# Kernel optimization log

Hardware: AMD Instinct MI355X
Metric: run time of the kernel (lower is better)

Reference implementation:

```python
import jax, jax.numpy as jnp
import numpy as np

B, S, H, I, E, TOPK = 4, 4096, 1024, 4096, 8, 2


def setup_inputs() -> dict:
    key = jax.random.key(0)
    k0, k1, k2, k3 = jax.random.split(key, 4)
    hidden_states = jax.random.normal(k0, (B, S, H), dtype=jnp.float32)
    # Router gate: Linear(hidden_size -> num_experts), no bias
    Wg = jax.random.normal(k1, (E, H), dtype=jnp.float32) * 0.02
    # Stacked per-expert FeedForward: w2(silu(w1(x)))
    W1 = jax.random.normal(k2, (E, I, H), dtype=jnp.float32) * 0.02
    b1 = jnp.zeros((E, I), dtype=jnp.float32)
    W2 = jax.random.normal(k3, (E, H, I), dtype=jnp.float32) * 0.02
    b2 = jnp.zeros((E, H), dtype=jnp.float32)
    return {"hidden_states": hidden_states, "Wg": Wg, "W1": W1, "b1": b1, "W2": W2, "b2": b2}


def _moe_forward(x, Wg, W1, b1, W2, b2):
    b, s, h = x.shape
    # Router: logits [B,S,E], softmax over experts, top-k, renormalize top-k weights
    logits = jnp.einsum("bsh,eh->bse", x, Wg)
    probs = jax.nn.softmax(logits, axis=-1)
    vals, idx = jax.lax.top_k(probs, TOPK)                      # [B,S,K]
    vals = vals / jnp.sum(vals, axis=-1, keepdims=True)
    # Dense combine weights [B,S,E] (E is small); zero for non-selected experts
    combine = jnp.sum(jax.nn.one_hot(idx, E, dtype=x.dtype) * vals[..., None], axis=-2)

    xf = x.reshape(b * s, h)                                    # [T,H]
    gate_te = combine.reshape(b * s, E).T                       # [E,T]

    def body(acc, xs):
        W1e, b1e, W2e, b2e, ge = xs
        hmid = jax.nn.silu(xf @ W1e.T + b1e)                    # [T,I]
        oe = hmid @ W2e.T + b2e                                 # [T,H]
        return acc + ge[:, None] * oe, None

    out, _ = jax.lax.scan(body, jnp.zeros_like(xf), (W1, b1, W2, b2, gate_te))
    return out.reshape(b, s, h), logits


def reference(hidden_states, Wg, W1, b1, W2, b2):
    return _moe_forward(hidden_states, Wg, W1, b1, W2, b2)
```

## Files before the change

### kernel.cpp

```cpp
#include <hip/hip_runtime.h>
#include <hip/hip_bf16.h>
#include <stdint.h>

#define T_TOK 16384
#define HDIM  1024
#define IDIM  4096
#define NEXP  8

typedef __bf16  bf16x8  __attribute__((ext_vector_type(8)));
typedef float   floatx4 __attribute__((ext_vector_type(4)));

__device__ __forceinline__ void gload16(const void* g, void* lds) {
  __builtin_amdgcn_global_load_lds(
      (__attribute__((address_space(1))) void*)g,
      (__attribute__((address_space(3))) void*)lds, 16, 0, 0);
}

__global__ __launch_bounds__(256) void cvtk(const float* __restrict__ s,
                                            __bf16* __restrict__ d, int n8) {
  int i = blockIdx.x * 256 + threadIdx.x;
  if (i >= n8) return;
  const float4* s4 = (const float4*)s;
  float4 a = s4[2 * i], b = s4[2 * i + 1];
  bf16x8 v;
  v[0] = (__bf16)a.x; v[1] = (__bf16)a.y; v[2] = (__bf16)a.z; v[3] = (__bf16)a.w;
  v[4] = (__bf16)b.x; v[5] = (__bf16)b.y; v[6] = (__bf16)b.z; v[7] = (__bf16)b.w;
  *(bf16x8*)(d + (size_t)i * 8) = v;
}

__global__ __launch_bounds__(256) void routerk(const float* __restrict__ x,
    const float* __restrict__ Wg, float* __restrict__ logits,
    int* __restrict__ topk_e, float* __restrict__ topk_g,
    int* __restrict__ gcount) {
  __shared__ int hist[NEXP];
  int tid = threadIdx.x;
  if (tid < NEXP) hist[tid] = 0;
  __syncthreads();
  int wv = tid >> 6, ln = tid & 63;
  for (int it = 0; it < 16; ++it) {
    int t = blockIdx.x * 64 + wv * 16 + it;
    const float* xr = x + (size_t)t * HDIM;
    float acc[NEXP];
#pragma unroll
    for (int e = 0; e < NEXP; e++) acc[e] = 0.f;
    for (int h = ln; h < HDIM; h += 64) {
      float xv = xr[h];
#pragma unroll
      for (int e = 0; e < NEXP; e++) acc[e] += xv * Wg[e * HDIM + h];
    }
#pragma unroll
    for (int e = 0; e < NEXP; e++) {
#pragma unroll
      for (int off = 32; off > 0; off >>= 1) acc[e] += __shfl_down(acc[e], off);
    }
    if (ln == 0) {
#pragma unroll
      for (int e = 0; e < NEXP; e++) logits[(size_t)t * NEXP + e] = acc[e];
      int i0 = 0;
#pragma unroll
      for (int e = 1; e < NEXP; e++) if (acc[e] > acc[i0]) i0 = e;
      int i1 = (i0 == 0) ? 1 : 0;
#pragma unroll
      for (int e = 0; e < NEXP; e++)
        if (e != i0 && e != i1 && acc[e] > acc[i1]) i1 = e;
      float r = expf(acc[i1] - acc[i0]);
      float s = 1.f + r;
      topk_e[2 * t] = i0;     topk_g[2 * t] = 1.f / s;
      topk_e[2 * t + 1] = i1; topk_g[2 * t + 1] = r / s;
      atomicAdd(&hist[i0], 1);
      atomicAdd(&hist[i1], 1);
    }
  }
  __syncthreads();
  if (tid < NEXP) atomicAdd(&gcount[tid], hist[tid]);
}

__global__ void prefixk(const int* __restrict__ gcount, int* __restrict__ goff,
                        int* __restrict__ gcur, int* __restrict__ tbl,
                        int* __restrict__ ntb, int CH) {
  if (threadIdx.x != 0 || blockIdx.x != 0) return;
  int s = 0;
  for (int g = 0; g < NEXP; g++) { goff[g] = s; gcur[g] = s; s += gcount[g]; }
  goff[NEXP] = s;
  int chunk_rows = (2 * T_TOK) / CH;
  int cnt[16];
  for (int c = 0; c < CH; c++) cnt[c] = 0;
  for (int g = 0; g < NEXP; g++) {
    int Ne = goff[g + 1] - goff[g];
    int nb = (Ne + 127) >> 7;
    for (int b = 0; b < nb; b++) {
      int gr0 = goff[g] + b * 128;
      int c = gr0 / chunk_rows;
      tbl[c * 288 + cnt[c]] = (g << 8) | b;
      cnt[c]++;
    }
  }
  for (int c = 0; c < CH; c++) ntb[c] = cnt[c];
}

__global__ __launch_bounds__(256) void scatterk(const int* __restrict__ topk_e,
    const float* __restrict__ topk_g, int* __restrict__ gcur,
    int* __restrict__ row_info, float* __restrict__ row_gate) {
  __shared__ int hist[NEXP];
  __shared__ int bbase[NEXP];
  int tid = threadIdx.x;
  if (tid < NEXP) hist[tid] = 0;
  __syncthreads();
  int t = blockIdx.x * 256 + tid;
  int e0 = topk_e[2 * t], e1 = topk_e[2 * t + 1];
  float g0 = topk_g[2 * t], g1 = topk_g[2 * t + 1];
  int l0 = atomicAdd(&hist[e0], 1);
  int l1 = atomicAdd(&hist[e1], 1);
  __syncthreads();
  if (tid < NEXP) bbase[tid] = atomicAdd(&gcur[tid], hist[tid]);
  __syncthreads();
  int p0 = bbase[e0] + l0;
  row_info[p0] = t; row_gate[p0] = g0;
  int p1 = bbase[e1] + l1;
  row_info[p1] = t; row_gate[p1] = g1;
}

__global__ __launch_bounds__(256) void gemm1k(
    const __bf16* __restrict__ xb, const __bf16* __restrict__ w1b,
    const float* __restrict__ b1, __bf16* __restrict__ hmid,
    const int* __restrict__ row_info, const int* __restrict__ goff,
    const int* __restrict__ tbl, const int* __restrict__ ntb, int chunk_base) {
  __shared__ __attribute__((aligned(16))) char smem[32768];
  if ((int)blockIdx.x >= ntb[0]) return;
  int info = tbl[blockIdx.x];
  int g = info >> 8, br = info & 255;
  int base = goff[g];
  int Ne = goff[g + 1] - base;
  int r0 = br * 128;
  if (r0 >= Ne) return;
  int n0 = blockIdx.y * 128;
  int tid = threadIdx.x, w = tid >> 6, ln = tid & 63;
  int ra = w * 32 + (ln >> 2);
  int ca = (ln & 3) * 16;
  int rA0 = r0 + ra;      if (rA0 > Ne - 1) rA0 = Ne - 1;
  int rA1 = r0 + ra + 16; if (rA1 > Ne - 1) rA1 = Ne - 1;
  int t0 = row_info[base + rA0];
  int t1 = row_info[base + rA1];
  const char* gA0 = (const char*)(xb + (size_t)t0 * HDIM) + ca;
  const char* gA1 = (const char*)(xb + (size_t)t1 * HDIM) + ca;
  const char* gB0 = (const char*)(w1b + (size_t)g * IDIM * HDIM + (size_t)(n0 + ra) * HDIM) + ca;
  const char* gB1 = (const char*)(w1b + (size_t)g * IDIM * HDIM + (size_t)(n0 + ra + 16) * HDIM) + ca;
  int aoff = w * 2048;
  int boff = 8192 + w * 2048;
  int lm = ln & 15, lq = ln >> 4;
  int rdA = ((w >> 1) * 64 + lm) * 64 + lq * 16;
  int rdB = 8192 + ((w & 1) * 64 + lm) * 64 + lq * 16;
  floatx4 acc[4][4] = {};
  gload16(gA0, smem + aoff);
  gload16(gA1, smem + aoff + 1024);
  gload16(gB0, smem + boff);
  gload16(gB1, smem + boff + 1024);
  const int NK = HDIM / 32;
  for (int kt = 0; kt < NK; kt++) {
    char* cbuf = smem + (kt & 1) * 16384;
    char* nbuf = smem + ((kt + 1) & 1) * 16384;
    __syncthreads();
    if (kt + 1 < NK) {
      int kb = (kt + 1) * 64;
      gload16(gA0 + kb, nbuf + aoff);
      gload16(gA1 + kb, nbuf + aoff + 1024);
      gload16(gB0 + kb, nbuf + boff);
      gload16(gB1 + kb, nbuf + boff + 1024);
    }
    bf16x8 af[4], bfv[4];
#pragma unroll
    for (int mi = 0; mi < 4; mi++) af[mi] = *(const bf16x8*)(cbuf + rdA + mi * 1024);
#pragma unroll
    for (int ni = 0; ni < 4; ni++) bfv[ni] = *(const bf16x8*)(cbuf + rdB + ni * 1024);
#pragma unroll
    for (int mi = 0; mi < 4; mi++)
#pragma unroll
      for (int ni = 0; ni < 4; ni++)
        acc[mi][ni] = __builtin_amdgcn_mfma_f32_16x16x32_bf16(af[mi], bfv[ni], acc[mi][ni], 0, 0, 0);
  }
  int colbase = n0 + (w & 1) * 64;
#pragma unroll
  for (int mi = 0; mi < 4; mi++) {
#pragma unroll
    for (int reg = 0; reg < 4; reg++) {
      int rr = r0 + (w >> 1) * 64 + mi * 16 + lq * 4 + reg;
      if (rr < Ne) {
        __bf16* orow = hmid + (size_t)(base + rr - chunk_base) * IDIM;
#pragma unroll
        for (int ni = 0; ni < 4; ni++) {
          int c = colbase + ni * 16 + lm;
          float v = acc[mi][ni][reg] + b1[g * IDIM + c];
          v = v / (1.f + __expf(-v));
          orow[c] = (__bf16)v;
        }
      }
    }
  }
}

__global__ __launch_bounds__(256) void gemm2k(
    const __bf16* __restrict__ hmid, const __bf16* __restrict__ w2b,
    const float* __restrict__ b2, float* __restrict__ out,
    const int* __restrict__ row_info, const float* __restrict__ row_gate,
    const int* __restrict__ goff, const int* __restrict__ tbl,
    const int* __restrict__ ntb, int chunk_base) {
  __shared__ __attribute__((aligned(16))) char smem[32768];
  if ((int)blockIdx.x >= ntb[0]) return;
  int info = tbl[blockIdx.x];
  int g = info >> 8, br = info & 255;
  int base = goff[g];
  int Ne = goff[g + 1] - base;
  int r0 = br * 128;
  if (r0 >= Ne) return;
  int n0 = blockIdx.y * 128;
  int tid = threadIdx.x, w = tid >> 6, ln = tid & 63;
  int ra = w * 32 + (ln >> 2);
  int ca = (ln & 3) * 16;
  int rA0 = r0 + ra;      if (rA0 > Ne - 1) rA0 = Ne - 1;
  int rA1 = r0 + ra + 16; if (rA1 > Ne - 1) rA1 = Ne - 1;
  const char* gA0 = (const char*)(hmid + (size_t)(base + rA0 - chunk_base) * IDIM) + ca;
  const char* gA1 = (const char*)(hmid + (size_t)(base + rA1 - chunk_base) * IDIM) + ca;
  const char* gB0 = (const char*)(w2b + (size_t)g * HDIM * IDIM + (size_t)(n0 + ra) * IDIM) + ca;
  const char* gB1 = (const char*)(w2b + (size_t)g * HDIM * IDIM + (size_t)(n0 + ra + 16) * IDIM) + ca;
  int aoff = w * 2048;
  int boff = 8192 + w * 2048;
  int lm = ln & 15, lq = ln >> 4;
  int rdA = ((w >> 1) * 64 + lm) * 64 + lq * 16;
  int rdB = 8192 + ((w & 1) * 64 + lm) * 64 + lq * 16;
  floatx4 acc[4][4] = {};
  gload16(gA0, smem + aoff);
  gload16(gA1, smem + aoff + 1024);
  gload16(gB0, smem + boff);
  gload16(gB1, smem + boff + 1024);
  const int NK = IDIM / 32;
  for (int kt = 0; kt < NK; kt++) {
    char* cbuf = smem + (kt & 1) * 16384;
    char* nbuf = smem + ((kt + 1) & 1) * 16384;
    __syncthreads();
    if (kt + 1 < NK) {
      int kb = (kt + 1) * 64;
      gload16(gA0 + kb, nbuf + aoff);
      gload16(gA1 + kb, nbuf + aoff + 1024);
      gload16(gB0 + kb, nbuf + boff);
      gload16(gB1 + kb, nbuf + boff + 1024);
    }
    bf16x8 af[4], bfv[4];
#pragma unroll
    for (int mi = 0; mi < 4; mi++) af[mi] = *(const bf16x8*)(cbuf + rdA + mi * 1024);
#pragma unroll
    for (int ni = 0; ni < 4; ni++) bfv[ni] = *(const bf16x8*)(cbuf + rdB + ni * 1024);
#pragma unroll
    for (int mi = 0; mi < 4; mi++)
#pragma unroll
      for (int ni = 0; ni < 4; ni++)
        acc[mi][ni] = __builtin_amdgcn_mfma_f32_16x16x32_bf16(af[mi], bfv[ni], acc[mi][ni], 0, 0, 0);
  }
  int colbase = n0 + (w & 1) * 64;
#pragma unroll
  for (int mi = 0; mi < 4; mi++) {
#pragma unroll
    for (int reg = 0; reg < 4; reg++) {
      int rr = r0 + (w >> 1) * 64 + mi * 16 + lq * 4 + reg;
      if (rr < Ne) {
        int t = row_info[base + rr];
        float gate = row_gate[base + rr];
        float* orow = out + (size_t)t * HDIM;
#pragma unroll
        for (int ni = 0; ni < 4; ni++) {
          int c = colbase + ni * 16 + lm;
          float v = gate * (acc[mi][ni][reg] + b2[g * HDIM + c]);
          atomicAdd(&orow[c], v);
        }
      }
    }
  }
}

extern "C" void kernel_launch(void* const* d_in, const int* in_sizes, int n_in,
                              void* d_out, int out_size, void* d_ws, size_t ws_size,
                              hipStream_t stream) {
  (void)in_sizes; (void)n_in; (void)out_size;
  const float* x  = (const float*)d_in[0];
  const float* Wg = (const float*)d_in[1];
  const float* W1 = (const float*)d_in[2];
  const float* b1 = (const float*)d_in[3];
  const float* W2 = (const float*)d_in[4];
  const float* b2 = (const float*)d_in[5];
  float* out = (float*)d_out;
  float* logits = out + (size_t)T_TOK * HDIM;

  const size_t xb_b   = (size_t)T_TOK * HDIM * 2;
  const size_t w_b    = (size_t)NEXP * IDIM * HDIM * 2;
  const size_t side_b = (size_t)2 * T_TOK * 4;
  const size_t meta_b = 32768;
  int CH = 2;
  while (CH < 16) {
    size_t hm = ((size_t)((2 * T_TOK) / CH) + 128) * IDIM * 2;
    size_t need = xb_b + 2 * w_b + hm + 4 * side_b + meta_b + 8192;
    if (need <= ws_size) break;
    CH *= 2;
  }
  const int R = (2 * T_TOK) / CH;

  char* p = (char*)d_ws;
  size_t off = 0;
  auto take = [&](size_t bytes) -> char* {
    char* r = p + off;
    off = (off + bytes + 255) & ~(size_t)255;
    return r;
  };
  __bf16* xb   = (__bf16*)take(xb_b);
  __bf16* w1b  = (__bf16*)take(w_b);
  __bf16* w2b  = (__bf16*)take(w_b);
  __bf16* hmid = (__bf16*)take(((size_t)R + 128) * IDIM * 2);
  int*   topk_e   = (int*)take(side_b);
  float* topk_g   = (float*)take(side_b);
  int*   row_info = (int*)take(side_b);
  float* row_gate = (float*)take(side_b);
  int*   gcount   = (int*)take(16 * 4);
  int*   goff     = (int*)take(17 * 4);
  int*   gcur     = (int*)take(16 * 4);
  int*   ntb      = (int*)take(16 * 4);
  int*   tbl      = (int*)take(16 * 288 * 4);

  hipMemsetAsync(gcount, 0, 16 * 4, stream);
  hipMemsetAsync(out, 0, (size_t)T_TOK * HDIM * 4, stream);

  cvtk<<<(T_TOK * HDIM / 8) / 256, 256, 0, stream>>>(x, xb, T_TOK * HDIM / 8);
  cvtk<<<(NEXP * IDIM * HDIM / 8) / 256, 256, 0, stream>>>(W1, w1b, NEXP * IDIM * HDIM / 8);
  cvtk<<<(NEXP * IDIM * HDIM / 8) / 256, 256, 0, stream>>>(W2, w2b, NEXP * IDIM * HDIM / 8);
  routerk<<<T_TOK / 64, 256, 0, stream>>>(x, Wg, logits, topk_e, topk_g, gcount);
  prefixk<<<1, 64, 0, stream>>>(gcount, goff, gcur, tbl, ntb, CH);
  scatterk<<<T_TOK / 256, 256, 0, stream>>>(topk_e, topk_g, gcur, row_info, row_gate);

  int gx = R / 128 + 8;
  for (int c = 0; c < CH; c++) {
    gemm1k<<<dim3(gx, IDIM / 128, 1), 256, 0, stream>>>(
        xb, w1b, b1, hmid, row_info, goff, tbl + c * 288, ntb + c, c * R);
    gemm2k<<<dim3(gx, HDIM / 128, 1), 256, 0, stream>>>(
        hmid, w2b, b2, out, row_info, row_gate, goff, tbl + c * 288, ntb + c, c * R);
  }
}
```

Measured before the change: 1.519 ms.

## Enlarge MoE GEMM tiles to 256x256 with 4-stage swizzled LDS pipeline

```diff
diff --git a/kernel.cpp b/kernel.cpp
--- a/kernel.cpp
+++ b/kernel.cpp
@@ -87,9 +87,9 @@
   for (int c = 0; c < CH; c++) cnt[c] = 0;
   for (int g = 0; g < NEXP; g++) {
     int Ne = goff[g + 1] - goff[g];
-    int nb = (Ne + 127) >> 7;
+    int nb = (Ne + 255) >> 8;
     for (int b = 0; b < nb; b++) {
-      int gr0 = goff[g] + b * 128;
+      int gr0 = goff[g] + b * 256;
       int c = gr0 / chunk_rows;
       tbl[c * 288 + cnt[c]] = (g << 8) | b;
       cnt[c]++;
@@ -120,70 +120,102 @@
   row_info[p1] = t; row_gate[p1] = g1;
 }
 
-__global__ __launch_bounds__(256) void gemm1k(
+
+__global__ __launch_bounds__(512, 2) void gemm1k(
     const __bf16* __restrict__ xb, const __bf16* __restrict__ w1b,
     const float* __restrict__ b1, __bf16* __restrict__ hmid,
     const int* __restrict__ row_info, const int* __restrict__ goff,
     const int* __restrict__ tbl, const int* __restrict__ ntb, int chunk_base) {
-  __shared__ __attribute__((aligned(16))) char smem[32768];
+  __shared__ __attribute__((aligned(16))) char smem[131072];
   if ((int)blockIdx.x >= ntb[0]) return;
   int info = tbl[blockIdx.x];
   int g = info >> 8, br = info & 255;
   int base = goff[g];
   int Ne = goff[g + 1] - base;
-  int r0 = br * 128;
+  int r0 = br * 256;
   if (r0 >= Ne) return;
-  int n0 = blockIdx.y * 128;
-  int tid = threadIdx.x, w = tid >> 6, ln = tid & 63;
-  int ra = w * 32 + (ln >> 2);
-  int ca = (ln & 3) * 16;
-  int rA0 = r0 + ra;      if (rA0 > Ne - 1) rA0 = Ne - 1;
-  int rA1 = r0 + ra + 16; if (rA1 > Ne - 1) rA1 = Ne - 1;
-  int t0 = row_info[base + rA0];
-  int t1 = row_info[base + rA1];
-  const char* gA0 = (const char*)(xb + (size_t)t0 * HDIM) + ca;
-  const char* gA1 = (const char*)(xb + (size_t)t1 * HDIM) + ca;
-  const char* gB0 = (const char*)(w1b + (size_t)g * IDIM * HDIM + (size_t)(n0 + ra) * HDIM) + ca;
-  const char* gB1 = (const char*)(w1b + (size_t)g * IDIM * HDIM + (size_t)(n0 + ra + 16) * HDIM) + ca;
-  int aoff = w * 2048;
-  int boff = 8192 + w * 2048;
+  int n0 = blockIdx.y * 256;
+  int tid = threadIdx.x, wid = tid >> 6, ln = tid & 63;
+  int wm = wid >> 2, wn = wid & 3;
   int lm = ln & 15, lq = ln >> 4;
-  int rdA = ((w >> 1) * 64 + lm) * 64 + lq * 16;
-  int rdB = 8192 + ((w & 1) * 64 + lm) * 64 + lq * 16;
-  floatx4 acc[4][4] = {};
-  gload16(gA0, smem + aoff);
-  gload16(gA1, smem + aoff + 1024);
-  gload16(gB0, smem + boff);
-  gload16(gB1, smem + boff + 1024);
-  const int NK = HDIM / 32;
-  for (int kt = 0; kt < NK; kt++) {
-    char* cbuf = smem + (kt & 1) * 16384;
-    char* nbuf = smem + ((kt + 1) & 1) * 16384;
-    __syncthreads();
-    if (kt + 1 < NK) {
-      int kb = (kt + 1) * 64;
-      gload16(gA0 + kb, nbuf + aoff);
-      gload16(gA1 + kb, nbuf + aoff + 1024);
-      gload16(gB0 + kb, nbuf + boff);
-      gload16(gB1 + kb, nbuf + boff + 1024);
-    }
-    bf16x8 af[4], bfv[4];
-#pragma unroll
-    for (int mi = 0; mi < 4; mi++) af[mi] = *(const bf16x8*)(cbuf + rdA + mi * 1024);
-#pragma unroll
-    for (int ni = 0; ni < 4; ni++) bfv[ni] = *(const bf16x8*)(cbuf + rdB + ni * 1024);
-#pragma unroll
-    for (int mi = 0; mi < 4; mi++)
-#pragma unroll
-      for (int ni = 0; ni < 4; ni++)
-        acc[mi][ni] = __builtin_amdgcn_mfma_f32_16x16x32_bf16(af[mi], bfv[ni], acc[mi][ni], 0, 0, 0);
-  }
-  int colbase = n0 + (w & 1) * 64;
-#pragma unroll
-  for (int mi = 0; mi < 4; mi++) {
+
+  int rb = tid >> 2;
+  int srcs = ((tid & 3) ^ ((tid >> 3) & 3)) * 16;
+  const char* gA[2]; const char* gB[2];
+#pragma unroll
+  for (int r = 0; r < 2; r++) {
+    int row = r0 + r * 128 + rb;
+    int rc = row < Ne ? row : Ne - 1;
+    int tk = row_info[base + rc];
+    gA[r] = (const char*)(xb + (size_t)tk * HDIM) + srcs;
+    gB[r] = (const char*)(w1b + (size_t)g * IDIM * HDIM +
+                          (size_t)(n0 + r * 128 + rb) * HDIM) + srcs;
+  }
+  int swz = (lq ^ ((lm >> 1) & 3)) * 16;
+  int rdA = (wm * 128 + lm) * 64 + swz;
+  int rdB = 16384 + (wn * 64 + lm) * 64 + swz;
+
+  floatx4 acc[8][4] = {};
+
+#define STAGE_A1(T) { int b_ = (T) & 3; size_t ko = (size_t)(T) * 64; \
+    gload16(gA[0] + ko, smem + b_ * 32768 + tid * 16); \
+    gload16(gA[1] + ko, smem + b_ * 32768 + 8192 + tid * 16); }
+#define STAGE_B1(T) { int b_ = (T) & 3; size_t ko = (size_t)(T) * 64; \
+    gload16(gB[0] + ko, smem + b_ * 32768 + 16384 + tid * 16); \
+    gload16(gB[1] + ko, smem + b_ * 32768 + 24576 + tid * 16); }
+
+  const int NT = HDIM / 32;
+#pragma unroll
+  for (int p = 0; p < 3; p++) { STAGE_A1(p); STAGE_B1(p); }
+
+#pragma unroll 1
+  for (int t = 0; t < NT; t++) {
+    bool st = (t < NT - 3);
+    if (st) STAGE_A1(t + 3);
+    int rem = NT - 1 - t;
+    if (rem >= 3)      asm volatile("s_waitcnt vmcnt(10)" ::: "memory");
+    else if (rem == 2) asm volatile("s_waitcnt vmcnt(8)" ::: "memory");
+    else if (rem == 1) asm volatile("s_waitcnt vmcnt(4)" ::: "memory");
+    else               asm volatile("s_waitcnt vmcnt(0)" ::: "memory");
+    __builtin_amdgcn_s_barrier();
+    asm volatile("" ::: "memory");
+    const char* cb = smem + (t & 3) * 32768;
+    bf16x8 af[8], bf[2];
+#pragma unroll
+    for (int mi = 0; mi < 8; mi++) af[mi] = *(const bf16x8*)(cb + rdA + mi * 1024);
+#pragma unroll
+    for (int ni = 0; ni < 2; ni++) bf[ni] = *(const bf16x8*)(cb + rdB + ni * 1024);
+    __builtin_amdgcn_s_setprio(1);
+#pragma unroll
+    for (int mi = 0; mi < 8; mi++)
+#pragma unroll
+      for (int ni = 0; ni < 2; ni++)
+        acc[mi][ni] = __builtin_amdgcn_mfma_f32_16x16x32_bf16(af[mi], bf[ni], acc[mi][ni], 0, 0, 0);
+    __builtin_amdgcn_s_setprio(0);
+    if (st) STAGE_B1(t + 3);
+    bf16x8 bg[2];
+#pragma unroll
+    for (int ni = 0; ni < 2; ni++) bg[ni] = *(const bf16x8*)(cb + rdB + (2 + ni) * 1024);
+    __builtin_amdgcn_s_setprio(1);
+#pragma unroll
+    for (int mi = 0; mi < 8; mi++)
+#pragma unroll
+      for (int ni = 0; ni < 2; ni++)
+        acc[mi][2 + ni] = __builtin_amdgcn_mfma_f32_16x16x32_bf16(af[mi], bg[ni], acc[mi][2 + ni], 0, 0, 0);
+    __builtin_amdgcn_s_setprio(0);
+    asm volatile("" ::: "memory");
+    __builtin_amdgcn_s_barrier();
+    asm volatile("" ::: "memory");
+  }
+#undef STAGE_A1
+#undef STAGE_B1
+
+  int colbase = n0 + wn * 64;
+#pragma unroll
+  for (int mi = 0; mi < 8; mi++) {
 #pragma unroll
     for (int reg = 0; reg < 4; reg++) {
-      int rr = r0 + (w >> 1) * 64 + mi * 16 + lq * 4 + reg;
+      int rr = r0 + wm * 128 + mi * 16 + lq * 4 + reg;
       if (rr < Ne) {
         __bf16* orow = hmid + (size_t)(base + rr - chunk_base) * IDIM;
 #pragma unroll
@@ -198,69 +230,100 @@
   }
 }
 
-__global__ __launch_bounds__(256) void gemm2k(
+__global__ __launch_bounds__(512, 2) void gemm2k(
     const __bf16* __restrict__ hmid, const __bf16* __restrict__ w2b,
     const float* __restrict__ b2, float* __restrict__ out,
     const int* __restrict__ row_info, const float* __restrict__ row_gate,
     const int* __restrict__ goff, const int* __restrict__ tbl,
     const int* __restrict__ ntb, int chunk_base) {
-  __shared__ __attribute__((aligned(16))) char smem[32768];
+  __shared__ __attribute__((aligned(16))) char smem[131072];
   if ((int)blockIdx.x >= ntb[0]) return;
   int info = tbl[blockIdx.x];
   int g = info >> 8, br = info & 255;
   int base = goff[g];
   int Ne = goff[g + 1] - base;
-  int r0 = br * 128;
+  int r0 = br * 256;
   if (r0 >= Ne) return;
-  int n0 = blockIdx.y * 128;
-  int tid = threadIdx.x, w = tid >> 6, ln = tid & 63;
-  int ra = w * 32 + (ln >> 2);
-  int ca = (ln & 3) * 16;
-  int rA0 = r0 + ra;      if (rA0 > Ne - 1) rA0 = Ne - 1;
-  int rA1 = r0 + ra + 16; if (rA1 > Ne - 1) rA1 = Ne - 1;
-  const char* gA0 = (const char*)(hmid + (size_t)(base + rA0 - chunk_base) * IDIM) + ca;
-  const char* gA1 = (const char*)(hmid + (size_t)(base + rA1 - chunk_base) * IDIM) + ca;
-  const char* gB0 = (const char*)(w2b + (size_t)g * HDIM * IDIM + (size_t)(n0 + ra) * IDIM) + ca;
-  const char* gB1 = (const char*)(w2b + (size_t)g * HDIM * IDIM + (size_t)(n0 + ra + 16) * IDIM) + ca;
-  int aoff = w * 2048;
-  int boff = 8192 + w * 2048;
+  int n0 = blockIdx.y * 256;
+  int tid = threadIdx.x, wid = tid >> 6, ln = tid & 63;
+  int wm = wid >> 2, wn = wid & 3;
   int lm = ln & 15, lq = ln >> 4;
-  int rdA = ((w >> 1) * 64 + lm) * 64 + lq * 16;
-  int rdB = 8192 + ((w & 1) * 64 + lm) * 64 + lq * 16;
-  floatx4 acc[4][4] = {};
-  gload16(gA0, smem + aoff);
-  gload16(gA1, smem + aoff + 1024);
-  gload16(gB0, smem + boff);
-  gload16(gB1, smem + boff + 1024);
-  const int NK = IDIM / 32;
-  for (int kt = 0; kt < NK; kt++) {
-    char* cbuf = smem + (kt & 1) * 16384;
-    char* nbuf = smem + ((kt + 1) & 1) * 16384;
-    __syncthreads();
-    if (kt + 1 < NK) {
-      int kb = (kt + 1) * 64;
-      gload16(gA0 + kb, nbuf + aoff);
-      gload16(gA1 + kb, nbuf + aoff + 1024);
-      gload16(gB0 + kb, nbuf + boff);
-      gload16(gB1 + kb, nbuf + boff + 1024);
-    }
-    bf16x8 af[4], bfv[4];
-#pragma unroll
-    for (int mi = 0; mi < 4; mi++) af[mi] = *(const bf16x8*)(cbuf + rdA + mi * 1024);
-#pragma unroll
-    for (int ni = 0; ni < 4; ni++) bfv[ni] = *(const bf16x8*)(cbuf + rdB + ni * 1024);
-#pragma unroll
-    for (int mi = 0; mi < 4; mi++)
-#pragma unroll
-      for (int ni = 0; ni < 4; ni++)
-        acc[mi][ni] = __builtin_amdgcn_mfma_f32_16x16x32_bf16(af[mi], bfv[ni], acc[mi][ni], 0, 0, 0);
-  }
-  int colbase = n0 + (w & 1) * 64;
-#pragma unroll
-  for (int mi = 0; mi < 4; mi++) {
+
+  int rb = tid >> 2;
+  int srcs = ((tid & 3) ^ ((tid >> 3) & 3)) * 16;
+  const char* gA[2]; const char* gB[2];
+#pragma unroll
+  for (int r = 0; r < 2; r++) {
+    int row = r0 + r * 128 + rb;
+    gA[r] = (const char*)(hmid + (size_t)(base + row - chunk_base) * IDIM) + srcs;
+    gB[r] = (const char*)(w2b + (size_t)g * HDIM * IDIM +
+                          (size_t)(n0 + r * 128 + rb) * IDIM) + srcs;
+  }
+  int swz = (lq ^ ((lm >> 1) & 3)) * 16;
+  int rdA = (wm * 128 + lm) * 64 + swz;
+  int rdB = 16384 + (wn * 64 + lm) * 64 + swz;
+
+  floatx4 acc[8][4] = {};
+
+#define STAGE_A2(T) { int b_ = (T) & 3; size_t ko = (size_t)(T) * 64; \
+    gload16(gA[0] + ko, smem + b_ * 32768 + tid * 16); \
+    gload16(gA[1] + ko, smem + b_ * 32768 + 8192 + tid * 16); }
+#define STAGE_B2(T) { int b_ = (T) & 3; size_t ko = (size_t)(T) * 64; \
+    gload16(gB[0] + ko, smem + b_ * 32768 + 16384 + tid * 16); \
+    gload16(gB[1] + ko, smem + b_ * 32768 + 24576 + tid * 16); }
+
+  const int NT = IDIM / 32;
+#pragma unroll
+  for (int p = 0; p < 3; p++) { STAGE_A2(p); STAGE_B2(p); }
+
+#pragma unroll 1
+  for (int t = 0; t < NT; t++) {
+    bool st = (t < NT - 3);
+    if (st) STAGE_A2(t + 3);
+    int rem = NT - 1 - t;
+    if (rem >= 3)      asm volatile("s_waitcnt vmcnt(10)" ::: "memory");
+    else if (rem == 2) asm volatile("s_waitcnt vmcnt(8)" ::: "memory");
+    else if (rem == 1) asm volatile("s_waitcnt vmcnt(4)" ::: "memory");
+    else               asm volatile("s_waitcnt vmcnt(0)" ::: "memory");
+    __builtin_amdgcn_s_barrier();
+    asm volatile("" ::: "memory");
+    const char* cb = smem + (t & 3) * 32768;
+    bf16x8 af[8], bf[2];
+#pragma unroll
+    for (int mi = 0; mi < 8; mi++) af[mi] = *(const bf16x8*)(cb + rdA + mi * 1024);
+#pragma unroll
+    for (int ni = 0; ni < 2; ni++) bf[ni] = *(const bf16x8*)(cb + rdB + ni * 1024);
+    __builtin_amdgcn_s_setprio(1);
+#pragma unroll
+    for (int mi = 0; mi < 8; mi++)
+#pragma unroll
+      for (int ni = 0; ni < 2; ni++)
+        acc[mi][ni] = __builtin_amdgcn_mfma_f32_16x16x32_bf16(af[mi], bf[ni], acc[mi][ni], 0, 0, 0);
+    __builtin_amdgcn_s_setprio(0);
+    if (st) STAGE_B2(t + 3);
+    bf16x8 bg[2];
+#pragma unroll
+    for (int ni = 0; ni < 2; ni++) bg[ni] = *(const bf16x8*)(cb + rdB + (2 + ni) * 1024);
+    __builtin_amdgcn_s_setprio(1);
+#pragma unroll
+    for (int mi = 0; mi < 8; mi++)
+#pragma unroll
+      for (int ni = 0; ni < 2; ni++)
+        acc[mi][2 + ni] = __builtin_amdgcn_mfma_f32_16x16x32_bf16(af[mi], bg[ni], acc[mi][2 + ni], 0, 0, 0);
+    __builtin_amdgcn_s_setprio(0);
+    asm volatile("" ::: "memory");
+    __builtin_amdgcn_s_barrier();
+    asm volatile("" ::: "memory");
+  }
+#undef STAGE_A2
+#undef STAGE_B2
+
+  int colbase = n0 + wn * 64;
+#pragma unroll
+  for (int mi = 0; mi < 8; mi++) {
 #pragma unroll
     for (int reg = 0; reg < 4; reg++) {
-      int rr = r0 + (w >> 1) * 64 + mi * 16 + lq * 4 + reg;
+      int rr = r0 + wm * 128 + mi * 16 + lq * 4 + reg;
       if (rr < Ne) {
         int t = row_info[base + rr];
         float gate = row_gate[base + rr];
@@ -295,7 +358,7 @@
   const size_t meta_b = 32768;
   int CH = 2;
   while (CH < 16) {
-    size_t hm = ((size_t)((2 * T_TOK) / CH) + 128) * IDIM * 2;
+    size_t hm = ((size_t)((2 * T_TOK) / CH) + 256) * IDIM * 2;
     size_t need = xb_b + 2 * w_b + hm + 4 * side_b + meta_b + 8192;
     if (need <= ws_size) break;
     CH *= 2;
@@ -312,7 +375,7 @@
   __bf16* xb   = (__bf16*)take(xb_b);
   __bf16* w1b  = (__bf16*)take(w_b);
   __bf16* w2b  = (__bf16*)take(w_b);
-  __bf16* hmid = (__bf16*)take(((size_t)R + 128) * IDIM * 2);
+  __bf16* hmid = (__bf16*)take(((size_t)R + 256) * IDIM * 2);
   int*   topk_e   = (int*)take(side_b);
   float* topk_g   = (float*)take(side_b);
   int*   row_info = (int*)take(side_b);
@@ -333,11 +396,11 @@
   prefixk<<<1, 64, 0, stream>>>(gcount, goff, gcur, tbl, ntb, CH);
   scatterk<<<T_TOK / 256, 256, 0, stream>>>(topk_e, topk_g, gcur, row_info, row_gate);
 
-  int gx = R / 128 + 8;
+  int gx = R / 256 + 8;
   for (int c = 0; c < CH; c++) {
-    gemm1k<<<dim3(gx, IDIM / 128, 1), 256, 0, stream>>>(
+    gemm1k<<<dim3(gx, IDIM / 256, 1), 512, 0, stream>>>(
         xb, w1b, b1, hmid, row_info, goff, tbl + c * 288, ntb + c, c * R);
-    gemm2k<<<dim3(gx, HDIM / 128, 1), 256, 0, stream>>>(
+    gemm2k<<<dim3(gx, HDIM / 256, 1), 512, 0, stream>>>(
         hmid, w2b, b2, out, row_info, row_gate, goff, tbl + c * 288, ntb + c, c * R);
   }
 }
```

New measurement: 1.585 ms. +4.4%, slower.
